# Performance work log

Hardware: AMD Instinct MI355X
Metric: run time of the kernel (lower is better)

The kernel has to match this reference:

```python
import jax, jax.numpy as jnp
import numpy as np

N_NODES = 100000
N_EDGES = 1600000
IN_DIM, HID_DIM, OUT_DIM = 128, 64, 32


def gcn_conv(x, edge_index, W, b, n_nodes):
    """PyG GCNConv: add self-loops, symmetric deg^-1/2 normalization,
    linear transform, gather->scatter-sum aggregation, then bias."""
    loops = jnp.arange(n_nodes, dtype=edge_index.dtype)
    src = jnp.concatenate([edge_index[0], loops])  # [E+N]
    dst = jnp.concatenate([edge_index[1], loops])  # [E+N]
    # degree over targets (includes self-loops)
    deg = jax.ops.segment_sum(jnp.ones_like(dst, dtype=x.dtype), dst,
                              num_segments=n_nodes)
    dinv = jnp.where(deg > 0, jax.lax.rsqrt(deg), 0.0)
    norm = dinv[src] * dinv[dst]                   # [E+N]
    h = x @ W                                      # [N, F_out]
    msg = h[src] * norm[:, None]                   # gather + scale
    out = jax.ops.segment_sum(msg, dst, num_segments=n_nodes)
    return out + b


def setup_inputs() -> dict:
    key = jax.random.key(0)
    k1, k2, k3, k4 = jax.random.split(key, 4)
    x = jax.random.normal(k1, (N_NODES, IN_DIM), dtype=jnp.float32)
    edge_index = jax.random.randint(k2, (2, N_EDGES), 0, N_NODES,
                                    dtype=jnp.int64)
    # Glorot-ish init for weights, zero bias (PyG default: glorot + zeros)
    W1 = jax.random.normal(k3, (IN_DIM, HID_DIM), dtype=jnp.float32) * (1.0 / np.sqrt(IN_DIM))
    b1 = jnp.zeros((HID_DIM,), dtype=jnp.float32)
    W2 = jax.random.normal(k4, (HID_DIM, OUT_DIM), dtype=jnp.float32) * (1.0 / np.sqrt(HID_DIM))
    b2 = jnp.zeros((OUT_DIM,), dtype=jnp.float32)
    return {"x": x, "edge_index": edge_index, "W1": W1, "b1": b1,
            "W2": W2, "b2": b2}


def reference(x, edge_index, W1, b1, W2, b2):
    n = x.shape[0]
    h = jax.nn.relu(gcn_conv(x, edge_index, W1, b1, n))
    return gcn_conv(h, edge_index, W2, b2, n)
```

## Files before the change

kernel.cpp:

```cpp
#include <hip/hip_runtime.h>


#define BLK 256
#define BLKC 1024
#define EPT 8
#define CITER 10
#define BSHIFT 9
#define NPB 512
#define SLOTB 10240
#define NBMAX 256

typedef unsigned int uint_t;
typedef unsigned short ushort_t;
typedef __attribute__((ext_vector_type(2))) float v2f;
typedef __attribute__((ext_vector_type(8))) short bf16x8;
typedef __attribute__((ext_vector_type(4))) float f32x4;

__device__ __forceinline__ uint_t pkbf(float lo, float hi) {
    uint_t r;
    asm("v_cvt_pk_bf16_f32 %0, %1, %2" : "=v"(r) : "v"(lo), "v"(hi));
    return r;
}

__device__ __forceinline__ void pkadd(v2f& a0, v2f& a1, v2f& a2, v2f& a3, uint4 v) {
    v2f p;
    p.x = __uint_as_float(v.x << 16); p.y = __uint_as_float(v.x & 0xffff0000u); a0 += p;
    p.x = __uint_as_float(v.y << 16); p.y = __uint_as_float(v.y & 0xffff0000u); a1 += p;
    p.x = __uint_as_float(v.z << 16); p.y = __uint_as_float(v.z & 0xffff0000u); a2 += p;
    p.x = __uint_as_float(v.w << 16); p.y = __uint_as_float(v.w & 0xffff0000u); a3 += p;
}

__device__ __forceinline__ bool detect64(const int* __restrict__ idx) {
    int z = 0;
#pragma unroll
    for (int i = 1; i < 32; i += 2) z |= idx[i];
    return z == 0;
}

__global__ void k_part(const int* __restrict__ idx, int* __restrict__ bcursor,
                       int* __restrict__ edge_part,
                       const float* __restrict__ W1, const float* __restrict__ W2,
                       ushort_t* __restrict__ wt, int E, int nbuck, int PB) {
    if (blockIdx.x == PB) {
        int t = threadIdx.x;
        int n = t >> 2, q = t & 3;
        uint_t buf[16];
#pragma unroll
        for (int i = 0; i < 16; ++i) {
            float a = W1[(size_t)(32 * q + 2 * i) * 64 + n];
            float b = W1[(size_t)(32 * q + 2 * i + 1) * 64 + n];
            buf[i] = pkbf(a, b);
        }
#pragma unroll
        for (int i = 0; i < 4; ++i)
            ((uint4*)wt)[(size_t)n * 16 + q * 4 + i] = *(uint4*)&buf[4 * i];
        if (t < 128) {
            int n2 = t >> 2, q2 = t & 3;
            uint_t b2[8];
#pragma unroll
            for (int i = 0; i < 8; ++i) {
                float a = W2[(size_t)(16 * q2 + 2 * i) * 32 + n2];
                float b = W2[(size_t)(16 * q2 + 2 * i + 1) * 32 + n2];
                b2[i] = pkbf(a, b);
            }
#pragma unroll
            for (int i = 0; i < 2; ++i)
                ((uint4*)(wt + 8192))[(size_t)n2 * 8 + q2 * 2 + i] = *(uint4*)&b2[4 * i];
        }
        return;
    }
    __shared__ int h[NBMAX];
    __shared__ int rb[NBMAX];
    bool is64 = detect64(idx);
    int t = threadIdx.x, blk = blockIdx.x;
    for (int i = t; i < nbuck; i += BLK) h[i] = 0;
    __syncthreads();
    int base = blk * (BLK * EPT) + t;
    int dst[EPT], src[EPT], rk[EPT];
#pragma unroll
    for (int k = 0; k < EPT; ++k) {
        int e = base + k * BLK;
        if (e < E) {
            if (is64) {
                uint2 dv = ((const uint2*)idx)[(size_t)E + e];
                uint2 sv = ((const uint2*)idx)[e];
                dst[k] = (int)dv.x;
                src[k] = (int)sv.x;
            } else {
                dst[k] = idx[E + e];
                src[k] = idx[e];
            }
            rk[k] = atomicAdd(&h[dst[k] >> BSHIFT], 1);
        } else {
            dst[k] = -1;
        }
    }
    __syncthreads();
    for (int i = t; i < nbuck; i += BLK) {
        int c = h[i];
        rb[i] = c ? atomicAdd(&bcursor[i], c) : 0;
    }
    __syncthreads();
#pragma unroll
    for (int k = 0; k < EPT; ++k) {
        if (dst[k] >= 0) {
            int b = dst[k] >> BSHIFT;
            edge_part[(size_t)b * SLOTB + rb[b] + rk[k]] =
                src[k] | ((dst[k] & (NPB - 1)) << 17);
        }
    }
}

__global__ __launch_bounds__(BLKC) void k_csr(
        const int* __restrict__ edge_part, const int* __restrict__ bcursor,
        int* __restrict__ row_ptr, int* __restrict__ deg, float* __restrict__ dinv,
        int* __restrict__ csr_src, int N, int nbuck) {
    __shared__ int cnt[NPB];
    __shared__ int off[NPB];
    __shared__ int wsum[8];
    int b = blockIdx.x, t = threadIdx.x;
    int node0 = b << BSHIFT;
    int nn = min(NPB, N - node0);
    int m = bcursor[b];
    size_t ebase = (size_t)b * SLOTB;
    if (t < NPB) cnt[t] = 0;
    __syncthreads();
    int pp[CITER], rr[CITER];
#pragma unroll
    for (int it = 0; it < CITER; ++it) {
        int e = t + it * BLKC;
        if (e < m) {
            int p = edge_part[ebase + e];
            pp[it] = p;
            rr[it] = atomicAdd(&cnt[((unsigned)p) >> 17], 1);
        }
    }
    __syncthreads();
    int cown = 0, xi = 0;
    if (t < NPB) {
        cown = cnt[t];
        xi = cown;
#pragma unroll
        for (int d = 1; d < 64; d <<= 1) {
            int y = __shfl_up(xi, d, 64);
            if ((t & 63) >= d) xi += y;
        }
        if ((t & 63) == 63) wsum[t >> 6] = xi;
    }
    __syncthreads();
    if (t < 8) {
        int wv = wsum[t];
#pragma unroll
        for (int d = 1; d < 8; d <<= 1) {
            int y = __shfl_up(wv, d, 64);
            if (t >= d) wv += y;
        }
        wsum[t] = wv;
    }
    __syncthreads();
    if (t < NPB) {
        int excl = xi - cown + ((t >= 64) ? wsum[(t >> 6) - 1] : 0);
        off[t] = excl;
        if (t < nn) {
            row_ptr[node0 + t] = (int)(ebase + excl);
            deg[node0 + t] = cown;
            dinv[node0 + t] = rsqrtf((float)(cown + 1));
        }
    }
    __syncthreads();
#pragma unroll
    for (int it = 0; it < CITER; ++it) {
        int e = t + it * BLKC;
        if (e < m) {
            int p = pp[it];
            int dlo = ((unsigned)p) >> 17;
            csr_src[ebase + off[dlo] + rr[it]] = p & 0x1FFFF;
        }
    }
}

__global__ __launch_bounds__(256) void k_gemm1(
        const float* __restrict__ x, const ushort_t* __restrict__ wt,
        const float* __restrict__ dinv, ushort_t* __restrict__ hs1, int N) {
    __shared__ ushort_t xb[64][136];
    __shared__ ushort_t wb[64][136];
    int t = threadIdx.x;
    int rbase = blockIdx.x * 64;
    if (blockIdx.x == 0 && t < 8) {
        uint4 z = {0u, 0u, 0u, 0u};
        ((uint4*)hs1)[(size_t)N * 8 + t] = z;
    }
    for (int i = t; i < 1024; i += BLK) {
        int n = i >> 4, q = i & 15;
        uint4 v = ((const uint4*)wt)[i];
        *(uint4*)&wb[n][8 * q] = v;
    }
    for (int i = t; i < 2048; i += BLK) {
        int r = i >> 5, c4 = i & 31;
        int rr = rbase + r; if (rr >= N) rr = N - 1;
        float4 v = ((const float4*)x)[(size_t)rr * 32 + c4];
        uint2 p;
        p.x = pkbf(v.x, v.y);
        p.y = pkbf(v.z, v.w);
        *(uint2*)&xb[r][4 * c4] = p;
    }
    __syncthreads();
    int w = t >> 6, l = t & 63;
    int lane16 = l & 15, quad = l >> 4;
    int mrow = 16 * w + lane16;
    f32x4 acc0 = {0.f, 0.f, 0.f, 0.f}, acc1 = {0.f, 0.f, 0.f, 0.f};
    f32x4 acc2 = {0.f, 0.f, 0.f, 0.f}, acc3 = {0.f, 0.f, 0.f, 0.f};
#pragma unroll
    for (int kk = 0; kk < 4; ++kk) {
        int k0 = kk * 32 + quad * 8;
        bf16x8 a  = *(const bf16x8*)&xb[mrow][k0];
        bf16x8 b0 = *(const bf16x8*)&wb[lane16][k0];
        bf16x8 b1 = *(const bf16x8*)&wb[lane16 + 16][k0];
        bf16x8 b2 = *(const bf16x8*)&wb[lane16 + 32][k0];
        bf16x8 b3 = *(const bf16x8*)&wb[lane16 + 48][k0];
        acc0 = __builtin_amdgcn_mfma_f32_16x16x32_bf16(a, b0, acc0, 0, 0, 0);
        acc1 = __builtin_amdgcn_mfma_f32_16x16x32_bf16(a, b1, acc1, 0, 0, 0);
        acc2 = __builtin_amdgcn_mfma_f32_16x16x32_bf16(a, b2, acc2, 0, 0, 0);
        acc3 = __builtin_amdgcn_mfma_f32_16x16x32_bf16(a, b3, acc3, 0, 0, 0);
    }
    __syncthreads();
    int orow = 16 * w + quad * 4;
    float d0 = dinv[min(rbase + orow + 0, N - 1)];
    float d1 = dinv[min(rbase + orow + 1, N - 1)];
    float d2 = dinv[min(rbase + orow + 2, N - 1)];
    float d3 = dinv[min(rbase + orow + 3, N - 1)];
    uint_t u;
    u = pkbf(acc0.x * d0, acc0.y * d1);
    xb[orow + 0][lane16] = (ushort_t)u;  xb[orow + 1][lane16] = (ushort_t)(u >> 16);
    u = pkbf(acc0.z * d2, acc0.w * d3);
    xb[orow + 2][lane16] = (ushort_t)u;  xb[orow + 3][lane16] = (ushort_t)(u >> 16);
    u = pkbf(acc1.x * d0, acc1.y * d1);
    xb[orow + 0][lane16 + 16] = (ushort_t)u;  xb[orow + 1][lane16 + 16] = (ushort_t)(u >> 16);
    u = pkbf(acc1.z * d2, acc1.w * d3);
    xb[orow + 2][lane16 + 16] = (ushort_t)u;  xb[orow + 3][lane16 + 16] = (ushort_t)(u >> 16);
    u = pkbf(acc2.x * d0, acc2.y * d1);
    xb[orow + 0][lane16 + 32] = (ushort_t)u;  xb[orow + 1][lane16 + 32] = (ushort_t)(u >> 16);
    u = pkbf(acc2.z * d2, acc2.w * d3);
    xb[orow + 2][lane16 + 32] = (ushort_t)u;  xb[orow + 3][lane16 + 32] = (ushort_t)(u >> 16);
    u = pkbf(acc3.x * d0, acc3.y * d1);
    xb[orow + 0][lane16 + 48] = (ushort_t)u;  xb[orow + 1][lane16 + 48] = (ushort_t)(u >> 16);
    u = pkbf(acc3.z * d2, acc3.w * d3);
    xb[orow + 2][lane16 + 48] = (ushort_t)u;  xb[orow + 3][lane16 + 48] = (ushort_t)(u >> 16);
    __syncthreads();
    for (int i = t; i < 512; i += BLK) {
        int r = i >> 3, c8 = i & 7;
        int rr = rbase + r;
        if (rr < N) {
            uint4 v = *(const uint4*)&xb[r][8 * c8];
            *(uint4*)&hs1[(size_t)rr * 64 + 8 * c8] = v;
        }
    }
}

__global__ void k_agg1(const uint_t* __restrict__ hs1, const int* __restrict__ row_ptr,
                       const int* __restrict__ deg, const int* __restrict__ csr_src,
                       const float* __restrict__ dinv, const float* __restrict__ b1,
                       ushort_t* __restrict__ a1b, int N) {
    int lane = threadIdx.x & 63;
    int g = lane >> 3;
    int c = lane & 7;
    int wavebase = ((blockIdx.x * blockDim.x + threadIdx.x) >> 6) * 8;
    int node = wavebase + g;
    bool alive = node < N;
    int nodeC = alive ? node : N - 1;
    const uint4* H = (const uint4*)hs1;
    float dn = dinv[nodeC];
    int beg = row_ptr[nodeC];
    int tot = alive ? deg[nodeC] : 0;
    uint4 selfv = H[(size_t)nodeC * 8 + c];
    int gbase = lane & 0x38;
    int wtot = tot;
    wtot = max(wtot, __shfl_xor(wtot, 8, 64));
    wtot = max(wtot, __shfl_xor(wtot, 16, 64));
    wtot = max(wtot, __shfl_xor(wtot, 32, 64));
    int nch = (wtot + 7) >> 3;
    v2f a0 = {0.f, 0.f}, a1_ = {0.f, 0.f}, a2 = {0.f, 0.f}, a3 = {0.f, 0.f};
    for (int i = 0; i < nch; ++i) {
        int base = 8 * i;
        int jal = (base + c < tot) ? csr_src[beg + base + c] : N;
        uint4 vv[8];
#pragma unroll
        for (int e = 0; e < 8; ++e) {
            int j = __shfl(jal, gbase + e, 64);
            vv[e] = H[(size_t)j * 8 + c];
        }
#pragma unroll
        for (int e = 0; e < 8; ++e)
            pkadd(a0, a1_, a2, a3, vv[e]);
    }
    pkadd(a0, a1_, a2, a3, selfv);
    if (alive) {
        const float4* B = (const float4*)b1;
        float4 bv0 = B[2 * c], bv1 = B[2 * c + 1];
        float o0 = fmaxf(fmaf(a0.x, dn, bv0.x), 0.f);
        float o1 = fmaxf(fmaf(a0.y, dn, bv0.y), 0.f);
        float o2 = fmaxf(fmaf(a1_.x, dn, bv0.z), 0.f);
        float o3 = fmaxf(fmaf(a1_.y, dn, bv0.w), 0.f);
        float o4 = fmaxf(fmaf(a2.x, dn, bv1.x), 0.f);
        float o5 = fmaxf(fmaf(a2.y, dn, bv1.y), 0.f);
        float o6 = fmaxf(fmaf(a3.x, dn, bv1.z), 0.f);
        float o7 = fmaxf(fmaf(a3.y, dn, bv1.w), 0.f);
        uint4 o;
        o.x = pkbf(o0, o1);
        o.y = pkbf(o2, o3);
        o.z = pkbf(o4, o5);
        o.w = pkbf(o6, o7);
        ((uint4*)a1b)[(size_t)node * 8 + c] = o;
    }
}

__global__ __launch_bounds__(256) void k_gemm2(
        const ushort_t* __restrict__ a1b, const ushort_t* __restrict__ wt,
        const float* __restrict__ dinv, ushort_t* __restrict__ hs2, int N) {
    __shared__ ushort_t ab[64][72];
    __shared__ ushort_t wb[32][72];
    int t = threadIdx.x;
    int rbase = blockIdx.x * 64;
    if (blockIdx.x == 0 && t < 4) {
        uint4 z = {0u, 0u, 0u, 0u};
        ((uint4*)hs2)[(size_t)N * 4 + t] = z;
    }
    for (int i = t; i < 256; i += BLK) {
        int n = i >> 3, q = i & 7;
        uint4 v = ((const uint4*)(wt + 8192))[i];
        *(uint4*)&wb[n][8 * q] = v;
    }
    for (int i = t; i < 512; i += BLK) {
        int r = i >> 3, c8 = i & 7;
        int rr = rbase + r; if (rr >= N) rr = N - 1;
        uint4 v = ((const uint4*)a1b)[(size_t)rr * 8 + c8];
        *(uint4*)&ab[r][8 * c8] = v;
    }
    __syncthreads();
    int w = t >> 6, l = t & 63;
    int lane16 = l & 15, quad = l >> 4;
    int mrow = 16 * w + lane16;
    f32x4 acc0 = {0.f, 0.f, 0.f, 0.f}, acc1 = {0.f, 0.f, 0.f, 0.f};
#pragma unroll
    for (int kk = 0; kk < 2; ++kk) {
        int k0 = kk * 32 + quad * 8;
        bf16x8 a  = *(const bf16x8*)&ab[mrow][k0];
        bf16x8 b0 = *(const bf16x8*)&wb[lane16][k0];
        bf16x8 b1 = *(const bf16x8*)&wb[lane16 + 16][k0];
        acc0 = __builtin_amdgcn_mfma_f32_16x16x32_bf16(a, b0, acc0, 0, 0, 0);
        acc1 = __builtin_amdgcn_mfma_f32_16x16x32_bf16(a, b1, acc1, 0, 0, 0);
    }
    __syncthreads();
    int orow = 16 * w + quad * 4;
    float d0 = dinv[min(rbase + orow + 0, N - 1)];
    float d1 = dinv[min(rbase + orow + 1, N - 1)];
    float d2 = dinv[min(rbase + orow + 2, N - 1)];
    float d3 = dinv[min(rbase + orow + 3, N - 1)];
    uint_t u;
    u = pkbf(acc0.x * d0, acc0.y * d1);
    ab[orow + 0][lane16] = (ushort_t)u;  ab[orow + 1][lane16] = (ushort_t)(u >> 16);
    u = pkbf(acc0.z * d2, acc0.w * d3);
    ab[orow + 2][lane16] = (ushort_t)u;  ab[orow + 3][lane16] = (ushort_t)(u >> 16);
    u = pkbf(acc1.x * d0, acc1.y * d1);
    ab[orow + 0][lane16 + 16] = (ushort_t)u;  ab[orow + 1][lane16 + 16] = (ushort_t)(u >> 16);
    u = pkbf(acc1.z * d2, acc1.w * d3);
    ab[orow + 2][lane16 + 16] = (ushort_t)u;  ab[orow + 3][lane16 + 16] = (ushort_t)(u >> 16);
    __syncthreads();
    for (int i = t; i < 256; i += BLK) {
        int r = i >> 2, c4 = i & 3;
        int rr = rbase + r;
        if (rr < N) {
            uint4 v = *(const uint4*)&ab[r][8 * c4];
            *(uint4*)&hs2[(size_t)rr * 32 + 8 * c4] = v;
        }
    }
}

__global__ void k_agg2(const uint_t* __restrict__ hs2, const int* __restrict__ row_ptr,
                       const int* __restrict__ deg, const int* __restrict__ csr_src,
                       const float* __restrict__ dinv, const float* __restrict__ b2,
                       float* __restrict__ out, int N) {
    int lane = threadIdx.x & 63;
    int g = lane >> 2;
    int c = lane & 3;
    int wavebase = ((blockIdx.x * blockDim.x + threadIdx.x) >> 6) * 16;
    int node = wavebase + g;
    bool alive = node < N;
    int nodeC = alive ? node : N - 1;
    const uint4* H = (const uint4*)hs2;
    float dn = dinv[nodeC];
    int beg = row_ptr[nodeC];
    int tot = alive ? deg[nodeC] : 0;
    uint4 selfv = H[(size_t)nodeC * 4 + c];
    int gbase = lane & 0x3C;
    int wtot = tot;
    wtot = max(wtot, __shfl_xor(wtot, 4, 64));
    wtot = max(wtot, __shfl_xor(wtot, 8, 64));
    wtot = max(wtot, __shfl_xor(wtot, 16, 64));
    wtot = max(wtot, __shfl_xor(wtot, 32, 64));
    int nch = (wtot + 3) >> 2;
    v2f a0 = {0.f, 0.f}, a1_ = {0.f, 0.f}, a2 = {0.f, 0.f}, a3 = {0.f, 0.f};
    for (int i = 0; i < nch; ++i) {
        int base = 4 * i;
        int jal = (base + c < tot) ? csr_src[beg + base + c] : N;
        uint4 vv[4];
#pragma unroll
        for (int e = 0; e < 4; ++e) {
            int j = __shfl(jal, gbase + e, 64);
            vv[e] = H[(size_t)j * 4 + c];
        }
#pragma unroll
        for (int e = 0; e < 4; ++e)
            pkadd(a0, a1_, a2, a3, vv[e]);
    }
    pkadd(a0, a1_, a2, a3, selfv);
    if (alive) {
        const float4* B = (const float4*)b2;
        float4 bv0 = B[2 * c], bv1 = B[2 * c + 1];
        float4 o0, o1;
        o0.x = fmaf(a0.x, dn, bv0.x);
        o0.y = fmaf(a0.y, dn, bv0.y);
        o0.z = fmaf(a1_.x, dn, bv0.z);
        o0.w = fmaf(a1_.y, dn, bv0.w);
        o1.x = fmaf(a2.x, dn, bv1.x);
        o1.y = fmaf(a2.y, dn, bv1.y);
        o1.z = fmaf(a3.x, dn, bv1.z);
        o1.w = fmaf(a3.y, dn, bv1.w);
        float4* O = (float4*)out;
        O[(size_t)node * 8 + 2 * c] = o0;
        O[(size_t)node * 8 + 2 * c + 1] = o1;
    }
}

extern "C" void kernel_launch(void* const* d_in, const int* in_sizes, int n_in,
                              void* d_out, int out_size, void* d_ws, size_t ws_size,
                              hipStream_t stream) {
    const float* x  = (const float*)d_in[0];
    const int*   idx = (const int*)d_in[1];
    const float* W1 = (const float*)d_in[2];
    const float* b1 = (const float*)d_in[3];
    const float* W2 = (const float*)d_in[4];
    const float* b2 = (const float*)d_in[5];
    float* out = (float*)d_out;

    const int N = in_sizes[0] / 128;
    const int E = in_sizes[1] / 2;
    const int nbuck = (N + NPB - 1) >> BSHIFT;
    const int PB = (E + BLK * EPT - 1) / (BLK * EPT);

    char* ws = (char*)d_ws;
    size_t off = 0;
    auto alloc = [&](size_t bytes) -> char* {
        char* p = ws + off;
        off = (off + bytes + 255) & ~(size_t)255;
        return p;
    };
    float* dinv     = (float*)alloc((size_t)N * 4);
    int*   row_ptr  = (int*)alloc((size_t)N * 4);
    int*   deg      = (int*)alloc((size_t)N * 4);
    int*   bcursor  = (int*)alloc((size_t)nbuck * 4);
    ushort_t* wt    = (ushort_t*)alloc((size_t)(8192 + 2048) * 2);
    int*   csr_src  = (int*)alloc((size_t)nbuck * SLOTB * 4);
    size_t ep_bytes = (size_t)nbuck * SLOTB * 4;
    size_t h1_bytes = (size_t)(N + 1) * 64 * 2;
    int*   edge_part = (int*)alloc(ep_bytes > h1_bytes ? ep_bytes : h1_bytes);
    ushort_t* a1b   = (ushort_t*)alloc((size_t)N * 64 * 2);
    ushort_t* hs1   = (ushort_t*)edge_part;
    ushort_t* hs2   = hs1;

    hipMemsetAsync(bcursor, 0, (size_t)nbuck * 4, stream);
    k_part<<<PB + 1, BLK, 0, stream>>>(idx, bcursor, edge_part, W1, W2, wt,
                                       E, nbuck, PB);
    k_csr<<<nbuck, BLKC, 0, stream>>>(edge_part, bcursor, row_ptr, deg, dinv,
                                      csr_src, N, nbuck);
    k_gemm1<<<(N + 63) / 64, BLK, 0, stream>>>(x, wt, dinv, hs1, N);
    k_agg1<<<(N * 8 + BLK - 1) / BLK, BLK, 0, stream>>>(
        (const uint_t*)hs1, row_ptr, deg, csr_src, dinv, b1, a1b, N);
    k_gemm2<<<(N + 63) / 64, BLK, 0, stream>>>(a1b, wt, dinv, hs2, N);
    k_agg2<<<(N * 4 + BLK - 1) / BLK, BLK, 0, stream>>>(
        (const uint_t*)hs2, row_ptr, deg, csr_src, dinv, b2, out, N);
}
```

Measured before the change: 207.5 us.

## Fuse layer-2 GEMM into layer-1 aggregation kernel via shared-memory MFMA

The layer-1 aggregation kernel now writes its ReLU'd bf16 rows to a 32-row shared tile and multiplies them by W2 with MFMA, scaling by dinv and storing hs2 directly. The separate k_gemm2 launch and the a1b intermediate round trip through global memory go away. In exchange each aggregation block needs extra __syncthreads and shared memory, and hs2 now gets its own buffer instead of aliasing hs1, which the fused kernel is still reading.

```diff
diff --git a/kernel.cpp b/kernel.cpp
--- a/kernel.cpp
+++ b/kernel.cpp
@@ -257,17 +257,31 @@
     }
 }
 
-__global__ void k_agg1(const uint_t* __restrict__ hs1, const int* __restrict__ row_ptr,
-                       const int* __restrict__ deg, const int* __restrict__ csr_src,
-                       const float* __restrict__ dinv, const float* __restrict__ b1,
-                       ushort_t* __restrict__ a1b, int N) {
-    int lane = threadIdx.x & 63;
+__global__ __launch_bounds__(256) void k_agg1(
+        const uint_t* __restrict__ hs1, const int* __restrict__ row_ptr,
+        const int* __restrict__ deg, const int* __restrict__ csr_src,
+        const float* __restrict__ dinv, const float* __restrict__ b1,
+        const ushort_t* __restrict__ wt, ushort_t* __restrict__ hs2, int N) {
+    __shared__ ushort_t ab[32][72];
+    __shared__ ushort_t wb2[32][72];
+    int t = threadIdx.x;
+    int lane = t & 63;
+    int w = t >> 6;
     int g = lane >> 3;
     int c = lane & 7;
-    int wavebase = ((blockIdx.x * blockDim.x + threadIdx.x) >> 6) * 8;
-    int node = wavebase + g;
+    int rbase = blockIdx.x * 32;
+    int node = rbase + w * 8 + g;
     bool alive = node < N;
     int nodeC = alive ? node : N - 1;
+    if (blockIdx.x == 0 && t < 4) {
+        uint4 z = {0u, 0u, 0u, 0u};
+        ((uint4*)hs2)[(size_t)N * 4 + t] = z;
+    }
+    {
+        int n = t >> 3, q = t & 7;
+        uint4 v = ((const uint4*)(wt + 8192))[t];
+        *(uint4*)&wb2[n][8 * q] = v;
+    }
     const uint4* H = (const uint4*)hs1;
     float dn = dinv[nodeC];
     int beg = row_ptr[nodeC];
@@ -294,84 +308,57 @@
             pkadd(a0, a1_, a2, a3, vv[e]);
     }
     pkadd(a0, a1_, a2, a3, selfv);
-    if (alive) {
+    {
         const float4* B = (const float4*)b1;
         float4 bv0 = B[2 * c], bv1 = B[2 * c + 1];
-        float o0 = fmaxf(fmaf(a0.x, dn, bv0.x), 0.f);
-        float o1 = fmaxf(fmaf(a0.y, dn, bv0.y), 0.f);
-        float o2 = fmaxf(fmaf(a1_.x, dn, bv0.z), 0.f);
-        float o3 = fmaxf(fmaf(a1_.y, dn, bv0.w), 0.f);
-        float o4 = fmaxf(fmaf(a2.x, dn, bv1.x), 0.f);
-        float o5 = fmaxf(fmaf(a2.y, dn, bv1.y), 0.f);
-        float o6 = fmaxf(fmaf(a3.x, dn, bv1.z), 0.f);
-        float o7 = fmaxf(fmaf(a3.y, dn, bv1.w), 0.f);
-        uint4 o;
-        o.x = pkbf(o0, o1);
-        o.y = pkbf(o2, o3);
-        o.z = pkbf(o4, o5);
-        o.w = pkbf(o6, o7);
-        ((uint4*)a1b)[(size_t)node * 8 + c] = o;
-    }
-}
-
-__global__ __launch_bounds__(256) void k_gemm2(
-        const ushort_t* __restrict__ a1b, const ushort_t* __restrict__ wt,
-        const float* __restrict__ dinv, ushort_t* __restrict__ hs2, int N) {
-    __shared__ ushort_t ab[64][72];
-    __shared__ ushort_t wb[32][72];
-    int t = threadIdx.x;
-    int rbase = blockIdx.x * 64;
-    if (blockIdx.x == 0 && t < 4) {
-        uint4 z = {0u, 0u, 0u, 0u};
-        ((uint4*)hs2)[(size_t)N * 4 + t] = z;
-    }
-    for (int i = t; i < 256; i += BLK) {
-        int n = i >> 3, q = i & 7;
-        uint4 v = ((const uint4*)(wt + 8192))[i];
-        *(uint4*)&wb[n][8 * q] = v;
-    }
-    for (int i = t; i < 512; i += BLK) {
-        int r = i >> 3, c8 = i & 7;
-        int rr = rbase + r; if (rr >= N) rr = N - 1;
-        uint4 v = ((const uint4*)a1b)[(size_t)rr * 8 + c8];
-        *(uint4*)&ab[r][8 * c8] = v;
-    }
-    __syncthreads();
-    int w = t >> 6, l = t & 63;
-    int lane16 = l & 15, quad = l >> 4;
-    int mrow = 16 * w + lane16;
-    f32x4 acc0 = {0.f, 0.f, 0.f, 0.f}, acc1 = {0.f, 0.f, 0.f, 0.f};
+        uint4 o = {0u, 0u, 0u, 0u};
+        if (alive) {
+            float o0 = fmaxf(fmaf(a0.x, dn, bv0.x), 0.f);
+            float o1 = fmaxf(fmaf(a0.y, dn, bv0.y), 0.f);
+            float o2 = fmaxf(fmaf(a1_.x, dn, bv0.z), 0.f);
+            float o3 = fmaxf(fmaf(a1_.y, dn, bv0.w), 0.f);
+            float o4 = fmaxf(fmaf(a2.x, dn, bv1.x), 0.f);
+            float o5 = fmaxf(fmaf(a2.y, dn, bv1.y), 0.f);
+            float o6 = fmaxf(fmaf(a3.x, dn, bv1.z), 0.f);
+            float o7 = fmaxf(fmaf(a3.y, dn, bv1.w), 0.f);
+            o.x = pkbf(o0, o1);
+            o.y = pkbf(o2, o3);
+            o.z = pkbf(o4, o5);
+            o.w = pkbf(o6, o7);
+        }
+        *(uint4*)&ab[w * 8 + g][8 * c] = o;
+    }
+    __syncthreads();
+    int lane16 = lane & 15, quad = lane >> 4;
+    int rt = w & 1, ct = w >> 1;
+    int mrow = 16 * rt + lane16;
+    f32x4 acc = {0.f, 0.f, 0.f, 0.f};
 #pragma unroll
     for (int kk = 0; kk < 2; ++kk) {
         int k0 = kk * 32 + quad * 8;
-        bf16x8 a  = *(const bf16x8*)&ab[mrow][k0];
-        bf16x8 b0 = *(const bf16x8*)&wb[lane16][k0];
-        bf16x8 b1 = *(const bf16x8*)&wb[lane16 + 16][k0];
-        acc0 = __builtin_amdgcn_mfma_f32_16x16x32_bf16(a, b0, acc0, 0, 0, 0);
-        acc1 = __builtin_amdgcn_mfma_f32_16x16x32_bf16(a, b1, acc1, 0, 0, 0);
-    }
-    __syncthreads();
-    int orow = 16 * w + quad * 4;
+        bf16x8 a = *(const bf16x8*)&ab[mrow][k0];
+        bf16x8 b = *(const bf16x8*)&wb2[16 * ct + lane16][k0];
+        acc = __builtin_amdgcn_mfma_f32_16x16x32_bf16(a, b, acc, 0, 0, 0);
+    }
+    __syncthreads();
+    int orow = 16 * rt + quad * 4;
+    int ocol = 16 * ct + lane16;
     float d0 = dinv[min(rbase + orow + 0, N - 1)];
     float d1 = dinv[min(rbase + orow + 1, N - 1)];
     float d2 = dinv[min(rbase + orow + 2, N - 1)];
     float d3 = dinv[min(rbase + orow + 3, N - 1)];
     uint_t u;
-    u = pkbf(acc0.x * d0, acc0.y * d1);
-    ab[orow + 0][lane16] = (ushort_t)u;  ab[orow + 1][lane16] = (ushort_t)(u >> 16);
-    u = pkbf(acc0.z * d2, acc0.w * d3);
-    ab[orow + 2][lane16] = (ushort_t)u;  ab[orow + 3][lane16] = (ushort_t)(u >> 16);
-    u = pkbf(acc1.x * d0, acc1.y * d1);
-    ab[orow + 0][lane16 + 16] = (ushort_t)u;  ab[orow + 1][lane16 + 16] = (ushort_t)(u >> 16);
-    u = pkbf(acc1.z * d2, acc1.w * d3);
-    ab[orow + 2][lane16 + 16] = (ushort_t)u;  ab[orow + 3][lane16 + 16] = (ushort_t)(u >> 16);
-    __syncthreads();
-    for (int i = t; i < 256; i += BLK) {
+    u = pkbf(acc.x * d0, acc.y * d1);
+    ab[orow + 0][ocol] = (ushort_t)u;  ab[orow + 1][ocol] = (ushort_t)(u >> 16);
+    u = pkbf(acc.z * d2, acc.w * d3);
+    ab[orow + 2][ocol] = (ushort_t)u;  ab[orow + 3][ocol] = (ushort_t)(u >> 16);
+    __syncthreads();
+    for (int i = t; i < 128; i += BLK) {
         int r = i >> 2, c4 = i & 3;
         int rr = rbase + r;
         if (rr < N) {
             uint4 v = *(const uint4*)&ab[r][8 * c4];
-            *(uint4*)&hs2[(size_t)rr * 32 + 8 * c4] = v;
+            ((uint4*)hs2)[(size_t)rr * 4 + c4] = v;
         }
     }
 }
@@ -464,9 +451,8 @@
     size_t ep_bytes = (size_t)nbuck * SLOTB * 4;
     size_t h1_bytes = (size_t)(N + 1) * 64 * 2;
     int*   edge_part = (int*)alloc(ep_bytes > h1_bytes ? ep_bytes : h1_bytes);
-    ushort_t* a1b   = (ushort_t*)alloc((size_t)N * 64 * 2);
+    ushort_t* hs2   = (ushort_t*)alloc((size_t)(N + 1) * 32 * 2);
     ushort_t* hs1   = (ushort_t*)edge_part;
-    ushort_t* hs2   = hs1;
 
     hipMemsetAsync(bcursor, 0, (size_t)nbuck * 4, stream);
     k_part<<<PB + 1, BLK, 0, stream>>>(idx, bcursor, edge_part, W1, W2, wt,
@@ -475,8 +461,7 @@
                                       csr_src, N, nbuck);
     k_gemm1<<<(N + 63) / 64, BLK, 0, stream>>>(x, wt, dinv, hs1, N);
     k_agg1<<<(N * 8 + BLK - 1) / BLK, BLK, 0, stream>>>(
-        (const uint_t*)hs1, row_ptr, deg, csr_src, dinv, b1, a1b, N);
-    k_gemm2<<<(N + 63) / 64, BLK, 0, stream>>>(a1b, wt, dinv, hs2, N);
+        (const uint_t*)hs1, row_ptr, deg, csr_src, dinv, b1, wt, hs2, N);
     k_agg2<<<(N * 4 + BLK - 1) / BLK, BLK, 0, stream>>>(
         (const uint_t*)hs2, row_ptr, deg, csr_src, dinv, b2, out, N);
 }
```

Result: faster. 200.3 us (median of 2 runs) (-3.4%).
